# Performance work log

Measured on AMD Instinct MI355X. Metric: run time of the kernel, lower is better.

## Reference

```python
import jax, jax.numpy as jnp
import numpy as np

HID, H, KVH, D = 4096, 32, 8, 128  # hidden_size, attn heads, kv heads, head_dim

def _rms_norm(x, w, eps):
    # x: [B, S, h, D]; normalize over last dim (dim 3 in torch code)
    var = jnp.mean(jnp.square(x), axis=-1, keepdims=True)
    return x * jax.lax.rsqrt(var + eps) * w

def _rotate_half(x):
    x1, x2 = jnp.split(x, 2, axis=-1)
    return jnp.concatenate((-x2, x1), axis=-1)

def _rope(x, cos, sin):
    return x * cos + _rotate_half(x) * sin

def setup_inputs() -> dict:
    key = jax.random.key(0)
    ks = jax.random.split(key, 10)
    B, S = 1, 2048
    return {
        'hidden_states': jax.random.normal(ks[0], (B, S, HID), jnp.float32),
        'cos': jax.random.uniform(ks[1], (1, 1, S, D), jnp.float32, -1.0, 1.0),
        'sin': jax.random.uniform(ks[2], (1, 1, S, D), jnp.float32, -1.0, 1.0),
        'wq': jax.random.normal(ks[3], (HID, H * D), jnp.float32) * 0.02,
        'wk': jax.random.normal(ks[4], (HID, KVH * D), jnp.float32) * 0.02,
        'wv': jax.random.normal(ks[5], (HID, KVH * D), jnp.float32) * 0.02,
        'wo': jax.random.normal(ks[6], (H * D, HID), jnp.float32) * 0.02,
        'q_norm_w': jnp.ones((D,), jnp.float32),
        'k_norm_w': jnp.ones((D,), jnp.float32),
        'eps': jnp.float32(1e-6),
    }

def reference(hidden_states, cos, sin, wq, wk, wv, wo, q_norm_w, k_norm_w, eps):
    B, S, _ = hidden_states.shape
    n_rep = H // KVH
    # projections + per-head RMSNorm (before transpose, over head_dim)
    q = _rms_norm((hidden_states @ wq).reshape(B, S, H, D), q_norm_w, eps)
    k = _rms_norm((hidden_states @ wk).reshape(B, S, KVH, D), k_norm_w, eps)
    v = (hidden_states @ wv).reshape(B, S, KVH, D)
    q = q.transpose(0, 2, 1, 3)  # [B,H,S,D]
    k = k.transpose(0, 2, 1, 3)  # [B,KVH,S,D]
    v = v.transpose(0, 2, 1, 3)
    q, k = _rope(q, cos, sin), _rope(k, cos, sin)
    # GQA repeat (equivalent to repeat_interleave on head dim)
    k = jnp.repeat(k, n_rep, axis=1)
    v = jnp.repeat(v, n_rep, axis=1)
    # NOTE: source computes self.scaling but never applies it; no causal mask applied.
    attn = jnp.einsum('bhqd,bhkd->bhqk', q, k)
    attn = jax.nn.softmax(attn.astype(jnp.float32), axis=-1)
    out = jnp.einsum('bhqk,bhkd->bhqd', attn, v)
    out = out.transpose(0, 2, 1, 3).reshape(B, S, H * D)
    return out @ wo
```

## Files before the change

### kernel.cpp

```cpp
#include <hip/hip_runtime.h>
#include <hip/hip_bf16.h>
#include <stdint.h>

#define SLEN 2048
#define HIDN 4096
#define NHEAD 32
#define NKV 8
#define HD 128
#define QKV_N 6144

typedef __hip_bfloat16 bf16;
typedef short short8 __attribute__((ext_vector_type(8)));
typedef _Float16 f16x8 __attribute__((ext_vector_type(8)));
typedef float f32x4 __attribute__((ext_vector_type(4)));
typedef float f32x16 __attribute__((ext_vector_type(16)));

__device__ __forceinline__ void gld16(const void* g, void* l) {
  __builtin_amdgcn_global_load_lds((const __attribute__((address_space(1))) void*)g,
                                   (__attribute__((address_space(3))) void*)l,
                                   16, 0, 0);
}

__device__ __forceinline__ unsigned short bfbits(float f) {
  bf16 h = __float2bfloat16(f);
  unsigned short u;
  __builtin_memcpy(&u, &h, 2);
  return u;
}
__device__ __forceinline__ unsigned int pack2(float a, float b) {
  return (unsigned int)bfbits(a) | ((unsigned int)bfbits(b) << 16);
}

__global__ __launch_bounds__(256) void gemm_kernel(
    const bf16* __restrict__ A, const bf16* __restrict__ B,
    float* __restrict__ C, int K, int lda, int ldb, int ldc)
{
  __shared__ __align__(16) bf16 smem[2 * 4096];
  bf16* sA = smem;
  bf16* sB = smem + 4096;

  const int nwg = gridDim.x * gridDim.y;
  int bid = blockIdx.y * gridDim.x + blockIdx.x;
  {
    const int q = nwg >> 3, rr = nwg & 7, x = bid & 7, idx = bid >> 3;
    bid = (x < rr ? x * (q + 1) : rr * (q + 1) + (x - rr) * q) + idx;
  }
  const int bx = bid % gridDim.x;
  const int by = bid / gridDim.x;
  const int row0 = by * 128;
  const int col0 = bx * 128;

  const int tid = threadIdx.x;
  const int w = tid >> 6;
  const int lane = tid & 63;
  const int wr = w >> 1, wc = w & 1;

  f32x4 acc[4][4] = {};
  const int fr = lane & 15;
  const int fk = (lane >> 4) << 3;

  const int nk = K >> 5;
  for (int kt = 0; kt < nk; ++kt) {
    const int k0 = kt << 5;
#pragma unroll
    for (int i = 0; i < 2; ++i) {
      const int grp = (i << 2) + w;
      const int c = grp * 64 + lane;
      const int r = c >> 2;
      const int kk = k0 + ((c & 3) << 3);
      gld16(A + (long)(row0 + r) * lda + kk, sA + grp * 512);
      gld16(B + (long)(col0 + r) * ldb + kk, sB + grp * 512);
    }
    __syncthreads();
    short8 a[4], b[4];
#pragma unroll
    for (int m = 0; m < 4; ++m) {
      a[m] = *(const short8*)(sA + (wr * 64 + m * 16 + fr) * 32 + fk);
      b[m] = *(const short8*)(sB + (wc * 64 + m * 16 + fr) * 32 + fk);
    }
    __builtin_amdgcn_s_setprio(1);
#pragma unroll
    for (int m = 0; m < 4; ++m)
#pragma unroll
      for (int n = 0; n < 4; ++n)
        acc[m][n] = __builtin_amdgcn_mfma_f32_16x16x32_bf16(a[m], b[n], acc[m][n], 0, 0, 0);
    __builtin_amdgcn_s_setprio(0);
    __syncthreads();
  }

  const int cr = (lane >> 4) << 2;
  const int cc = lane & 15;
#pragma unroll
  for (int m = 0; m < 4; ++m)
#pragma unroll
    for (int n = 0; n < 4; ++n)
#pragma unroll
      for (int r = 0; r < 4; ++r) {
        const long row = row0 + wr * 64 + m * 16 + cr + r;
        const long col = col0 + wc * 64 + n * 16 + cc;
        C[row * (long)ldc + col] = acc[m][n][r];
      }
}

__global__ __launch_bounds__(256) void transpose_kernel(
    const float* __restrict__ src, long srcZ, int srcLd,
    bf16* __restrict__ dst, long dstZ, int dstLd)
{
  __shared__ float t[64][65];
  const int z = blockIdx.z;
  src += (long)z * srcZ;
  const long db = (long)z * dstZ;
  const int k0 = blockIdx.x * 64;
  const int n0 = blockIdx.y * 64;
  const int tx = threadIdx.x & 63;
  const int ty = threadIdx.x >> 6;
#pragma unroll
  for (int r = ty; r < 64; r += 4)
    t[r][tx] = src[(long)(k0 + r) * srcLd + n0 + tx];
  __syncthreads();
#pragma unroll
  for (int r = ty; r < 64; r += 4)
    dst[db + (long)(n0 + r) * dstLd + k0 + tx] = __float2bfloat16(t[tx][r]);
}

__global__ __launch_bounds__(256) void cvt_bf16_kernel(
    const float* __restrict__ x, bf16* __restrict__ y, int n)
{
  const int i = (blockIdx.x * 256 + threadIdx.x) * 4;
  if (i >= n) return;
  const f32x4 v = *(const f32x4*)(x + i);
#pragma unroll
  for (int j = 0; j < 4; ++j) y[i + j] = __float2bfloat16(v[j]);
}

__global__ __launch_bounds__(256) void rope_norm_kernel(
    const float* __restrict__ x_, int ld, int nh,
    const float* __restrict__ nw, const float* __restrict__ cosb,
    const float* __restrict__ sinb, const float* __restrict__ epsp,
    _Float16* __restrict__ df)
{
  const int gw = blockIdx.x * 4 + (threadIdx.x >> 6);
  const int lane = threadIdx.x & 63;
  const int srow = gw / nh;
  const int head = gw - srow * nh;
  const float* x = x_ + (long)srow * ld + head * HD;
  const float x0 = x[lane];
  const float x1 = x[lane + 64];
  float ss = x0 * x0 + x1 * x1;
#pragma unroll
  for (int o = 32; o > 0; o >>= 1) ss += __shfl_xor(ss, o);
  const float rr = rsqrtf(ss * (1.0f / 128.0f) + epsp[0]);
  const float nv0 = x0 * rr * nw[lane];
  const float nv1 = x1 * rr * nw[lane + 64];
  const float c0 = cosb[srow * HD + lane];
  const float c1 = cosb[srow * HD + lane + 64];
  const float sn0 = sinb[srow * HD + lane];
  const float sn1 = sinb[srow * HD + lane + 64];
  const float o0 = nv0 * c0 - nv1 * sn0;
  const float o1 = nv1 * c1 + nv0 * sn1;
  const long base = ((long)head * SLEN + srow) * HD;
  df[base + lane] = (_Float16)o0;
  df[base + lane + 64] = (_Float16)o1;
}

__global__ __launch_bounds__(512, 2) void flash_kernel(
    const _Float16* __restrict__ qf, const _Float16* __restrict__ kf,
    const bf16* __restrict__ vt,
    bf16* __restrict__ AO)
{
  __shared__ __align__(16) _Float16 sK[2][64 * 128];
  __shared__ __align__(16) bf16 sV[2][64 * 128];
  __shared__ float sStat[8][32];

  const int lin = blockIdx.x;
  const int swz = (lin & 7) * 32 + (lin >> 3);
  const int kvh = swz >> 5;
  const int head = kvh * 4 + ((swz >> 3) & 3);
  const int qt = swz & 7;

  const int tid = threadIdx.x;
  const int w = tid >> 6;
  const int lane = tid & 63;
  const int q31 = lane & 31;
  const int hi = lane >> 5;

  f16x8 bq[8];
  {
    const long qb = ((long)head * SLEN + qt * 256 + w * 32 + q31) * HD + hi * 8;
#pragma unroll
    for (int ks = 0; ks < 8; ++ks)
      bq[ks] = *(const f16x8*)(qf + qb + ks * 16);
  }

  const _Float16* kb = kf + (long)kvh * SLEN * HD;
  const bf16* vb = vt + (long)kvh * HD * SLEN;

  auto stage = [&](int t, int buf) {
#pragma unroll
    for (int i = 0; i < 2; ++i) {
      const int c = i * 512 + tid;
      const int row = c >> 4;
      const int sg = (c & 15) ^ (row & 15);
      gld16(kb + (long)(t * 64 + row) * HD + sg * 8,
            (_Float16*)sK[buf] + (i * 512 + w * 64) * 8);
    }
#pragma unroll
    for (int i = 0; i < 2; ++i) {
      const int c = i * 512 + tid;
      const int rp = c >> 4;
      const int sg = (c & 15) ^ (rp & 15);
      const int d = rp * 2 + (sg >> 3);
      gld16(vb + (long)d * SLEN + t * 64 + (sg & 7) * 8,
            (bf16*)sV[buf] + (i * 512 + w * 64) * 8);
    }
  };

  f32x16 o[4] = {};
  float m = -3.0e38f, l = 0.0f;

  stage(0, 0);
  stage(1, 1);
  asm volatile("s_waitcnt vmcnt(4)" ::: "memory");
  __builtin_amdgcn_sched_barrier(0);
  __builtin_amdgcn_s_barrier();
  __builtin_amdgcn_sched_barrier(0);

  for (int t = 0; t < SLEN / 64; ++t) {
    const int cur = t & 1;
    const _Float16* K = sK[cur];
    const bf16* V = sV[cur];

    f32x16 s0 = {}, s1 = {};
    __builtin_amdgcn_s_setprio(1);
#pragma unroll
    for (int ks = 0; ks < 8; ++ks) {
      const int slot = (2 * ks + hi) ^ (q31 & 15);
      const f16x8 a0 = *(const f16x8*)(K + q31 * 128 + slot * 8);
      const f16x8 a1 = *(const f16x8*)(K + (32 + q31) * 128 + slot * 8);
      s0 = __builtin_amdgcn_mfma_f32_32x32x16_f16(a0, bq[ks], s0, 0, 0, 0);
      s1 = __builtin_amdgcn_mfma_f32_32x32x16_f16(a1, bq[ks], s1, 0, 0, 0);
    }
    __builtin_amdgcn_s_setprio(0);

    float pmax = s0[0];
#pragma unroll
    for (int r = 1; r < 16; ++r) pmax = fmaxf(pmax, s0[r]);
#pragma unroll
    for (int r = 0; r < 16; ++r) pmax = fmaxf(pmax, s1[r]);
    pmax = fmaxf(pmax, __shfl_xor(pmax, 32));

    if (!__all(pmax - m <= 8.0f)) {
      const float mnew = fmaxf(m, pmax);
      const float corr = __expf(m - mnew);
      m = mnew;
      l *= corr;
      sStat[w][q31] = corr;
      asm volatile("s_waitcnt lgkmcnt(0)" ::: "memory");
      __builtin_amdgcn_sched_barrier(0);
      f32x4 c4[4];
#pragma unroll
      for (int rr = 0; rr < 4; ++rr)
        c4[rr] = *(const f32x4*)&sStat[w][8 * rr + 4 * hi];
#pragma unroll
      for (int nt = 0; nt < 4; ++nt)
#pragma unroll
        for (int r = 0; r < 16; ++r) o[nt][r] *= c4[r >> 2][r & 3];
    }

    float psum = 0.0f;
#pragma unroll
    for (int r = 0; r < 16; ++r) { s0[r] = __expf(s0[r] - m); psum += s0[r]; }
#pragma unroll
    for (int r = 0; r < 16; ++r) { s1[r] = __expf(s1[r] - m); psum += s1[r]; }
    psum += __shfl_xor(psum, 32);
    l += psum;

    unsigned int pk[16], sw[16];
#pragma unroll
    for (int i = 0; i < 8; ++i) pk[i] = pack2(s0[2 * i], s0[2 * i + 1]);
#pragma unroll
    for (int i = 0; i < 8; ++i) pk[8 + i] = pack2(s1[2 * i], s1[2 * i + 1]);
#pragma unroll
    for (int i = 0; i < 16; ++i) sw[i] = __shfl_xor((int)pk[i], 32);

    short8 pa[4];
#pragma unroll
    for (int ks = 0; ks < 4; ++ks) {
      const int base = (ks >> 1) * 8 + (ks & 1) * 4 + 2 * hi;
      union { unsigned int u[4]; short8 v; } tu;
      if (hi == 0) {
        tu.u[0] = pk[base]; tu.u[1] = pk[base + 1];
        tu.u[2] = sw[base]; tu.u[3] = sw[base + 1];
      } else {
        tu.u[0] = sw[base]; tu.u[1] = sw[base + 1];
        tu.u[2] = pk[base]; tu.u[3] = pk[base + 1];
      }
      pa[ks] = tu.v;
    }

    __builtin_amdgcn_s_setprio(1);
#pragma unroll
    for (int nt = 0; nt < 4; ++nt) {
      const int d = nt * 32 + q31;
      const int rp = d >> 1;
      const int sbase = ((d & 1) << 3) + hi;
#pragma unroll
      for (int ks = 0; ks < 4; ++ks) {
        const int slot = (sbase + 2 * ks) ^ (rp & 15);
        const short8 bv = *(const short8*)(V + rp * 128 + slot * 8);
        o[nt] = __builtin_amdgcn_mfma_f32_32x32x16_bf16(pa[ks], bv, o[nt], 0, 0, 0);
      }
    }
    __builtin_amdgcn_s_setprio(0);

    __builtin_amdgcn_s_barrier();
    __builtin_amdgcn_sched_barrier(0);
    if (t + 2 < SLEN / 64) {
      stage(t + 2, cur);
      asm volatile("s_waitcnt vmcnt(4)" ::: "memory");
    } else {
      asm volatile("s_waitcnt vmcnt(0)" ::: "memory");
    }
    __builtin_amdgcn_sched_barrier(0);
    __builtin_amdgcn_s_barrier();
    __builtin_amdgcn_sched_barrier(0);
  }

  sStat[w][q31] = l;
  asm volatile("s_waitcnt lgkmcnt(0)" ::: "memory");
  __builtin_amdgcn_sched_barrier(0);
  f32x4 l4[4];
#pragma unroll
  for (int rr = 0; rr < 4; ++rr) {
    const f32x4 lv = *(const f32x4*)&sStat[w][8 * rr + 4 * hi];
#pragma unroll
    for (int j = 0; j < 4; ++j) l4[rr][j] = 1.0f / lv[j];
  }
#pragma unroll
  for (int nt = 0; nt < 4; ++nt)
#pragma unroll
    for (int rr = 0; rr < 4; ++rr)
#pragma unroll
      for (int j = 0; j < 4; ++j) {
        const long row = qt * 256 + w * 32 + 8 * rr + 4 * hi + j;
        AO[row * HIDN + head * 128 + nt * 32 + q31] =
            __float2bfloat16(o[nt][rr * 4 + j] * l4[rr][j]);
      }
}

extern "C" void kernel_launch(void* const* d_in, const int* in_sizes, int n_in,
                              void* d_out, int out_size, void* d_ws, size_t ws_size,
                              hipStream_t stream)
{
  const float* hs   = (const float*)d_in[0];
  const float* cosb = (const float*)d_in[1];
  const float* sinb = (const float*)d_in[2];
  const float* wq   = (const float*)d_in[3];
  const float* wk   = (const float*)d_in[4];
  const float* wv   = (const float*)d_in[5];
  const float* wo   = (const float*)d_in[6];
  const float* qw   = (const float*)d_in[7];
  const float* kw   = (const float*)d_in[8];
  const float* eps  = (const float*)d_in[9];

  const size_t MB = 1024 * 1024;
  if (ws_size < 116 * MB) return;
  uint8_t* ws = (uint8_t*)d_ws;

  bf16*  hsb = (bf16*)(ws + 0 * MB);
  bf16*  WT  = (bf16*)(ws + 16 * MB);
  float* QKV = (float*)(ws + 64 * MB);
  _Float16* qf = (_Float16*)(ws + 16 * MB);
  _Float16* kf = (_Float16*)(ws + 32 * MB);
  bf16*  Vt  = (bf16*)(ws + 36 * MB);
  bf16*  AO  = (bf16*)(ws + 64 * MB);
  bf16*  WoT = (bf16*)(ws + 80 * MB);

  cvt_bf16_kernel<<<SLEN * HIDN / 4 / 256, 256, 0, stream>>>(hs, hsb, SLEN * HIDN);

  transpose_kernel<<<dim3(64, 64, 1), 256, 0, stream>>>(wq, 0, HIDN, WT, 0, HIDN);
  transpose_kernel<<<dim3(64, 16, 1), 256, 0, stream>>>(wk, 0, 1024, WT + (size_t)4096 * HIDN, 0, HIDN);
  transpose_kernel<<<dim3(64, 16, 1), 256, 0, stream>>>(wv, 0, 1024, WT + (size_t)5120 * HIDN, 0, HIDN);

  gemm_kernel<<<dim3(48, 16, 1), 256, 0, stream>>>(hsb, WT, QKV, HIDN, HIDN, HIDN, QKV_N);

  rope_norm_kernel<<<SLEN * NHEAD / 4, 256, 0, stream>>>(QKV, QKV_N, NHEAD, qw, cosb, sinb, eps, qf);
  rope_norm_kernel<<<SLEN * NKV / 4, 256, 0, stream>>>(QKV + 4096, QKV_N, NKV, kw, cosb, sinb, eps, kf);

  transpose_kernel<<<dim3(32, 2, 8), 256, 0, stream>>>(QKV + 5120, 128, QKV_N, Vt, (long)HD * SLEN, SLEN);

  transpose_kernel<<<dim3(64, 64, 1), 256, 0, stream>>>(wo, 0, HIDN, WoT, 0, HIDN);

  flash_kernel<<<dim3(256, 1, 1), 512, 0, stream>>>(qf, kf, Vt, AO);

  gemm_kernel<<<dim3(32, 16, 1), 256, 0, stream>>>(AO, WoT, (float*)d_out, HIDN, HIDN, HIDN, HIDN);
}
```

Before: 478.3 us.

## Rewrite GEMM with 256x128 tiles, triple-buffered LDS and XOR swizzle

```diff
diff --git a/kernel.cpp b/kernel.cpp
--- a/kernel.cpp
+++ b/kernel.cpp
@@ -31,13 +31,12 @@
   return (unsigned int)bfbits(a) | ((unsigned int)bfbits(b) << 16);
 }
 
-__global__ __launch_bounds__(256) void gemm_kernel(
+__global__ __launch_bounds__(512) void gemm256_kernel(
     const bf16* __restrict__ A, const bf16* __restrict__ B,
     float* __restrict__ C, int K, int lda, int ldb, int ldc)
 {
-  __shared__ __align__(16) bf16 smem[2 * 4096];
-  bf16* sA = smem;
-  bf16* sB = smem + 4096;
+  __shared__ __align__(16) bf16 sA3[3][256 * 64];
+  __shared__ __align__(16) bf16 sB3[3][128 * 64];
 
   const int nwg = gridDim.x * gridDim.y;
   int bid = blockIdx.y * gridDim.x + blockIdx.x;
@@ -47,58 +46,124 @@
   }
   const int bx = bid % gridDim.x;
   const int by = bid / gridDim.x;
-  const int row0 = by * 128;
+  const int row0 = by * 256;
   const int col0 = bx * 128;
 
   const int tid = threadIdx.x;
   const int w = tid >> 6;
   const int lane = tid & 63;
-  const int wr = w >> 1, wc = w & 1;
+  const int wm = w >> 1;
+  const int wn = w & 1;
+  const int fr = lane & 15;
+  const int g = lane >> 4;
+
+  auto stage = [&](int t, int b) {
+    const int k0 = t << 6;
+#pragma unroll
+    for (int i = 0; i < 4; ++i) {
+      const int c = i * 512 + tid;
+      const int row = c >> 3;
+      const int slot = (c & 7) ^ (row & 7);
+      gld16(A + (long)(row0 + row) * lda + k0 + slot * 8,
+            (bf16*)sA3[b] + (i * 512 + w * 64 + lane) * 8 - lane * 8 + lane * 8);
+    }
+#pragma unroll
+    for (int i = 0; i < 2; ++i) {
+      const int c = i * 512 + tid;
+      const int row = c >> 3;
+      const int slot = (c & 7) ^ (row & 7);
+      gld16(B + (long)(col0 + row) * ldb + k0 + slot * 8,
+            (bf16*)sB3[b] + (i * 512 + w * 64 + lane) * 8 - lane * 8 + lane * 8);
+    }
+  };
 
   f32x4 acc[4][4] = {};
-  const int fr = lane & 15;
-  const int fk = (lane >> 4) << 3;
-
-  const int nk = K >> 5;
-  for (int kt = 0; kt < nk; ++kt) {
-    const int k0 = kt << 5;
-#pragma unroll
-    for (int i = 0; i < 2; ++i) {
-      const int grp = (i << 2) + w;
-      const int c = grp * 64 + lane;
-      const int r = c >> 2;
-      const int kk = k0 + ((c & 3) << 3);
-      gld16(A + (long)(row0 + r) * lda + kk, sA + grp * 512);
-      gld16(B + (long)(col0 + r) * ldb + kk, sB + grp * 512);
-    }
-    __syncthreads();
-    short8 a[4], b[4];
-#pragma unroll
-    for (int m = 0; m < 4; ++m) {
-      a[m] = *(const short8*)(sA + (wr * 64 + m * 16 + fr) * 32 + fk);
-      b[m] = *(const short8*)(sB + (wc * 64 + m * 16 + fr) * 32 + fk);
-    }
-    __builtin_amdgcn_s_setprio(1);
-#pragma unroll
-    for (int m = 0; m < 4; ++m)
-#pragma unroll
-      for (int n = 0; n < 4; ++n)
-        acc[m][n] = __builtin_amdgcn_mfma_f32_16x16x32_bf16(a[m], b[n], acc[m][n], 0, 0, 0);
-    __builtin_amdgcn_s_setprio(0);
-    __syncthreads();
+
+  const int nk = K >> 6;
+  stage(0, 0);
+  stage(1, 1);
+
+  for (int t = 0; t < nk; ++t) {
+    const int buf = t % 3;
+    __builtin_amdgcn_s_barrier();
+    __builtin_amdgcn_sched_barrier(0);
+    if (t + 2 < nk) {
+      stage(t + 2, (t + 2) % 3);
+      asm volatile("s_waitcnt vmcnt(12)" ::: "memory");
+    } else if (t + 2 == nk) {
+      asm volatile("s_waitcnt vmcnt(6)" ::: "memory");
+    } else {
+      asm volatile("s_waitcnt vmcnt(0)" ::: "memory");
+    }
+    __builtin_amdgcn_sched_barrier(0);
+    __builtin_amdgcn_s_barrier();
+    __builtin_amdgcn_sched_barrier(0);
+
+    const bf16* Ab = sA3[buf];
+    const bf16* Bb = sB3[buf];
+
+    short8 bfr[4][2];
+#pragma unroll
+    for (int nf = 0; nf < 4; ++nf)
+#pragma unroll
+      for (int ks = 0; ks < 2; ++ks) {
+        const int row = wn * 64 + nf * 16 + fr;
+        bfr[nf][ks] = *(const short8*)(Bb + row * 64 + ((ks * 4 + g) ^ (row & 7)) * 8);
+      }
+
+    {
+      short8 afr[2][2];
+#pragma unroll
+      for (int mf = 0; mf < 2; ++mf)
+#pragma unroll
+        for (int ks = 0; ks < 2; ++ks) {
+          const int row = wm * 64 + mf * 16 + fr;
+          afr[mf][ks] = *(const short8*)(Ab + row * 64 + ((ks * 4 + g) ^ (row & 7)) * 8);
+        }
+      __builtin_amdgcn_s_setprio(1);
+#pragma unroll
+      for (int mf = 0; mf < 2; ++mf)
+#pragma unroll
+        for (int nf = 0; nf < 4; ++nf)
+#pragma unroll
+          for (int ks = 0; ks < 2; ++ks)
+            acc[mf][nf] = __builtin_amdgcn_mfma_f32_16x16x32_bf16(
+                afr[mf][ks], bfr[nf][ks], acc[mf][nf], 0, 0, 0);
+      __builtin_amdgcn_s_setprio(0);
+    }
+    {
+      short8 afr[2][2];
+#pragma unroll
+      for (int mf = 0; mf < 2; ++mf)
+#pragma unroll
+        for (int ks = 0; ks < 2; ++ks) {
+          const int row = wm * 64 + (mf + 2) * 16 + fr;
+          afr[mf][ks] = *(const short8*)(Ab + row * 64 + ((ks * 4 + g) ^ (row & 7)) * 8);
+        }
+      __builtin_amdgcn_s_setprio(1);
+#pragma unroll
+      for (int mf = 0; mf < 2; ++mf)
+#pragma unroll
+        for (int nf = 0; nf < 4; ++nf)
+#pragma unroll
+          for (int ks = 0; ks < 2; ++ks)
+            acc[mf + 2][nf] = __builtin_amdgcn_mfma_f32_16x16x32_bf16(
+                afr[mf][ks], bfr[nf][ks], acc[mf + 2][nf], 0, 0, 0);
+      __builtin_amdgcn_s_setprio(0);
+    }
   }
 
-  const int cr = (lane >> 4) << 2;
-  const int cc = lane & 15;
-#pragma unroll
-  for (int m = 0; m < 4; ++m)
-#pragma unroll
-    for (int n = 0; n < 4; ++n)
+  const int cr = g << 2;
+  const int cc = fr;
+#pragma unroll
+  for (int mf = 0; mf < 4; ++mf)
+#pragma unroll
+    for (int nf = 0; nf < 4; ++nf)
 #pragma unroll
       for (int r = 0; r < 4; ++r) {
-        const long row = row0 + wr * 64 + m * 16 + cr + r;
-        const long col = col0 + wc * 64 + n * 16 + cc;
-        C[row * (long)ldc + col] = acc[m][n][r];
+        const long row = row0 + wm * 64 + mf * 16 + cr + r;
+        const long col = col0 + wn * 64 + nf * 16 + cc;
+        C[row * (long)ldc + col] = acc[mf][nf][r];
       }
 }
 
@@ -382,7 +447,7 @@
   transpose_kernel<<<dim3(64, 16, 1), 256, 0, stream>>>(wk, 0, 1024, WT + (size_t)4096 * HIDN, 0, HIDN);
   transpose_kernel<<<dim3(64, 16, 1), 256, 0, stream>>>(wv, 0, 1024, WT + (size_t)5120 * HIDN, 0, HIDN);
 
-  gemm_kernel<<<dim3(48, 16, 1), 256, 0, stream>>>(hsb, WT, QKV, HIDN, HIDN, HIDN, QKV_N);
+  gemm256_kernel<<<dim3(48, 8, 1), 512, 0, stream>>>(hsb, WT, QKV, HIDN, HIDN, HIDN, QKV_N);
 
   rope_norm_kernel<<<SLEN * NHEAD / 4, 256, 0, stream>>>(QKV, QKV_N, NHEAD, qw, cosb, sinb, eps, qf);
   rope_norm_kernel<<<SLEN * NKV / 4, 256, 0, stream>>>(QKV + 4096, QKV_N, NKV, kw, cosb, sinb, eps, kf);
@@ -393,5 +458,5 @@
 
   flash_kernel<<<dim3(256, 1, 1), 512, 0, stream>>>(qf, kf, Vt, AO);
 
-  gemm_kernel<<<dim3(32, 16, 1), 256, 0, stream>>>(AO, WoT, (float*)d_out, HIDN, HIDN, HIDN, HIDN);
-}
+  gemm256_kernel<<<dim3(32, 8, 1), 512, 0, stream>>>(AO, WoT, (float*)d_out, HIDN, HIDN, HIDN, HIDN);
+}
```

Measured after the change: 492.5 us. 1.03x slower.
